# Kernel optimization log

Hardware: AMD Instinct MI355X
Metric: run time of the kernel (lower is better)

## Reference

```python
import jax, jax.numpy as jnp
import numpy as np

B, N, D_MODEL, H = 4, 2048, 1024, 16  # batch, seq, model dim, heads


def setup_inputs() -> dict:
    key = jax.random.key(0)
    k1, k2, k3 = jax.random.split(key, 3)
    x = jax.random.normal(k1, (B, N, D_MODEL), dtype=jnp.float32)
    # nn.Linear weights: [out_features, in_features]; scaled for stability
    Wqkv = jax.random.normal(k2, (3 * D_MODEL, D_MODEL), dtype=jnp.float32) * 0.02
    bqkv = jnp.zeros((3 * D_MODEL,), dtype=jnp.float32)
    Wo = jax.random.normal(k3, (D_MODEL, D_MODEL), dtype=jnp.float32) * 0.02
    bo = jnp.zeros((D_MODEL,), dtype=jnp.float32)
    return {"x": x, "Wqkv": Wqkv, "bqkv": bqkv, "Wo": Wo, "bo": bo}


def reference(x, Wqkv, bqkv, Wo, bo):
    b, n, _ = x.shape
    qkv = x @ Wqkv.T + bqkv                      # [b, n, 3*d_model]
    # rearrange 'b n (h d) -> b h n d' with h heads, then chunk into q,k,v
    qkv = qkv.reshape(b, n, H, -1).transpose(0, 2, 1, 3)  # [b, h, n, 3*dh]
    q, k, v = jnp.split(qkv, 3, axis=-1)          # each [b, h, n, dh]
    scale = k.shape[-1] ** 0.5
    scores = jnp.einsum('bhqd,bhkd->bhqk', q, k) / scale
    attn = jax.nn.softmax(scores, axis=-1)
    out = jnp.einsum('bhqk,bhkd->bhqd', attn, v)  # [b, h, n, dh]
    out = out.transpose(0, 2, 1, 3).reshape(b, n, -1)  # 'b h n d -> b n (h d)'
    return out @ Wo.T + bo
```

## Files before the change

kernel.cpp:

```cpp
#include <hip/hip_runtime.h>
#include <hip/hip_bf16.h>

using bf16 = __hip_bfloat16;
typedef __attribute__((ext_vector_type(8))) __bf16 bf16x8;
typedef __attribute__((ext_vector_type(4))) float f32x4;
typedef __attribute__((ext_vector_type(16))) float f32x16;
typedef __attribute__((ext_vector_type(4))) unsigned u32x4;

#define MFMA16(a, b, c) __builtin_amdgcn_mfma_f32_16x16x32_bf16((a), (b), (c), 0, 0, 0)
#define MFMA32(a, b, c) __builtin_amdgcn_mfma_f32_32x32x16_bf16((a), (b), (c), 0, 0, 0)

#define WAITV4 asm volatile("s_waitcnt vmcnt(4)" ::: "memory")
#define WAITV2 asm volatile("s_waitcnt vmcnt(2)" ::: "memory")
#define WAITV0 asm volatile("s_waitcnt vmcnt(0)" ::: "memory")
#define WAITL0 asm volatile("s_waitcnt lgkmcnt(0)" ::: "memory")
#define BAR    __builtin_amdgcn_s_barrier()
#define SCHED0 __builtin_amdgcn_sched_barrier(0)

static __device__ __forceinline__ void gload_lds16(const bf16* g, bf16* l) {
    __builtin_amdgcn_global_load_lds(
        (__attribute__((address_space(1))) void*)(bf16*)(g),
        (__attribute__((address_space(3))) void*)(l), 16, 0, 0);
}

static __device__ __forceinline__ unsigned cvtpk(float lo, float hi) {
    unsigned r;
    asm("v_cvt_pk_bf16_f32 %0, %1, %2" : "=v"(r) : "v"(lo), "v"(hi));
    return r;
}

__global__ void cvt_all(const float* __restrict__ x, const float* __restrict__ wq,
                        const float* __restrict__ wo,
                        bf16* __restrict__ xb, bf16* __restrict__ wqb, bf16* __restrict__ wob) {
    int b = blockIdx.x;
    const float* src;
    bf16* dst;
    long i;
    if (b < 8192)       { src = x;  dst = xb;  i = (long)b * 256 + threadIdx.x; }
    else if (b < 11264) { src = wq; dst = wqb; i = (long)(b - 8192) * 256 + threadIdx.x; }
    else                { src = wo; dst = wob; i = (long)(b - 11264) * 256 + threadIdx.x; }
    float4 v = ((const float4*)src)[i];
    bf16 t[4];
    t[0] = __float2bfloat16(v.x);
    t[1] = __float2bfloat16(v.y);
    t[2] = __float2bfloat16(v.z);
    t[3] = __float2bfloat16(v.w);
    *(uint2*)(dst + 4l * i) = *(uint2*)t;
}


#define GEMM_STAGE(AB, BB, K0)                                             \
    do {                                                                   \
        gload_lds16(Ab + (long)srow * K + (K0) + scol, (AB) + t * 8);      \
        gload_lds16(Ab + (long)(srow + 64) * K + (K0) + scol, (AB) + 2048 + t * 8); \
        gload_lds16(Bb + (long)srow * K + (K0) + scol, (BB) + t * 8);      \
        gload_lds16(Bb + (long)(srow + 64) * K + (K0) + scol, (BB) + 2048 + t * 8); \
    } while (0)

#define GEMM_COMPUTE(AB, BB)                                               \
    do {                                                                   \
        bf16x8 af[4], bfv[4];                                              \
        _Pragma("unroll") for (int mi4 = 0; mi4 < 4; mi4++)                \
            af[mi4] = *(const bf16x8*)((AB) + (wm * 64 + mi4 * 16 + r) * 32 + q * 8); \
        _Pragma("unroll") for (int ni4 = 0; ni4 < 4; ni4++)                \
            bfv[ni4] = *(const bf16x8*)((BB) + (wn * 64 + ni4 * 16 + r) * 32 + q * 8); \
        __builtin_amdgcn_s_setprio(1);                                     \
        _Pragma("unroll") for (int mi4 = 0; mi4 < 4; mi4++)                \
            _Pragma("unroll") for (int ni4 = 0; ni4 < 4; ni4++)            \
                acc[mi4][ni4] = MFMA16(af[mi4], bfv[ni4], acc[mi4][ni4]);  \
        __builtin_amdgcn_s_setprio(0);                                     \
    } while (0)

#define GEMM_MAIN_LOOP                                                     \
    GEMM_STAGE(A0, B0, 0);                                                 \
    GEMM_STAGE(A1, B1, 32);                                                \
    for (int k0 = 0; k0 < K - 64; k0 += 64) {                              \
        WAITV4; BAR; SCHED0;                                               \
        GEMM_COMPUTE(A0, B0);                                              \
        WAITL0; BAR; SCHED0;                                               \
        GEMM_STAGE(A0, B0, k0 + 64);                                       \
        WAITV4; BAR; SCHED0;                                               \
        GEMM_COMPUTE(A1, B1);                                              \
        WAITL0; BAR; SCHED0;                                               \
        if (k0 + 96 < K) GEMM_STAGE(A1, B1, k0 + 96);                      \
    }                                                                      \
    WAITV4; BAR; SCHED0;                                                   \
    GEMM_COMPUTE(A0, B0);                                                  \
    WAITV0; BAR; SCHED0;                                                   \
    GEMM_COMPUTE(A1, B1);

__global__ void gemm_qkv(const bf16* __restrict__ A, const bf16* __restrict__ B,
                         const float* __restrict__ bias,
                         bf16* __restrict__ Qo, bf16* __restrict__ Ko, bf16* __restrict__ Vt) {
    const int K = 1024;
    __shared__ bf16 smem[16384];
    bf16* A0 = smem;
    bf16* B0 = smem + 4096;
    bf16* A1 = smem + 8192;
    bf16* B1 = smem + 12288;
    int t = threadIdx.x;
    int lane = t & 63;
    int wave = t >> 6;
    int wm = wave >> 1, wn = wave & 1;
    int r = lane & 15, q = lane >> 4;
    int lin = blockIdx.x;
    int xcd = lin & 7, rr_ = lin >> 3;
    int mi = xcd * 8 + rr_ / 24;
    int ni = rr_ % 24;
    long m0 = (long)mi * 128;
    long n0 = (long)ni * 128;
    const bf16* Ab = A + m0 * K;
    const bf16* Bb = B + n0 * K;

    f32x4 acc[4][4] = {};

    int srow = t >> 2;
    int scol = (t & 3) << 3;

    GEMM_MAIN_LOOP

#pragma unroll
    for (int ni4 = 0; ni4 < 4; ni4++) {
        int n = (int)n0 + wn * 64 + ni4 * 16 + r;
        float bn = bias[n];
        int h = n / 192;
        int rem = n % 192;
        int part = rem >> 6;
        int d = rem & 63;
#pragma unroll
        for (int mi4 = 0; mi4 < 4; mi4++) {
#pragma unroll
            for (int rr = 0; rr < 4; rr++) {
                int m = (int)m0 + wm * 64 + mi4 * 16 + q * 4 + rr;
                int b = m >> 11;
                int row = m & 2047;
                long bh = b * 16 + h;
                bf16 bv = __float2bfloat16(acc[mi4][ni4][rr] + bn);
                if (part == 0)      Qo[(bh * 2048 + row) * 64 + d] = bv;
                else if (part == 1) Ko[(bh * 2048 + row) * 64 + d] = bv;
                else                Vt[(bh * 64 + d) * 2048 + row] = bv;
            }
        }
    }
}


#define PACK8(S, OFF, OUTV) { \
    unsigned A0_ = cvtpk(S[OFF+0], S[OFF+1]); \
    unsigned B0_ = cvtpk(S[OFF+4], S[OFF+5]); \
    unsigned A1_ = cvtpk(S[OFF+2], S[OFF+3]); \
    unsigned B1_ = cvtpk(S[OFF+6], S[OFF+7]); \
    asm("v_permlane32_swap_b32 %0, %1" : "+v"(A0_), "+v"(B0_)); \
    asm("v_permlane32_swap_b32 %0, %1" : "+v"(A1_), "+v"(B1_)); \
    u32x4 W; W.x = A0_; W.y = A1_; W.z = B0_; W.w = B1_; \
    OUTV = __builtin_bit_cast(bf16x8, W); }

#define COMPUTE(KB, VB) do { \
    f32x16 sA = {}, sB = {}; \
    __builtin_amdgcn_s_setprio(1); \
    { \
        bf16x8 kA, kB; \
        kA = *(const bf16x8*)(KB + (0 * 64 + lane) * 8); \
        kB = *(const bf16x8*)(KB + (256 + 0 * 64 + lane) * 8); \
        sA = MFMA32(kA, qf0, sA);  sB = MFMA32(kB, qf0, sB); \
        kA = *(const bf16x8*)(KB + (1 * 64 + lane) * 8); \
        kB = *(const bf16x8*)(KB + (256 + 1 * 64 + lane) * 8); \
        sA = MFMA32(kA, qf1, sA);  sB = MFMA32(kB, qf1, sB); \
        kA = *(const bf16x8*)(KB + (2 * 64 + lane) * 8); \
        kB = *(const bf16x8*)(KB + (256 + 2 * 64 + lane) * 8); \
        sA = MFMA32(kA, qf2, sA);  sB = MFMA32(kB, qf2, sB); \
        kA = *(const bf16x8*)(KB + (3 * 64 + lane) * 8); \
        kB = *(const bf16x8*)(KB + (256 + 3 * 64 + lane) * 8); \
        sA = MFMA32(kA, qf3, sA);  sB = MFMA32(kB, qf3, sB); \
    } \
    __builtin_amdgcn_s_setprio(0); \
    float x0 = fmaxf(fmaxf(sA[0], sA[1]), fmaxf(sA[2], sA[3])); \
    float x1 = fmaxf(fmaxf(sA[4], sA[5]), fmaxf(sA[6], sA[7])); \
    float x2 = fmaxf(fmaxf(sA[8], sA[9]), fmaxf(sA[10], sA[11])); \
    float x3 = fmaxf(fmaxf(sA[12], sA[13]), fmaxf(sA[14], sA[15])); \
    float y0 = fmaxf(fmaxf(sB[0], sB[1]), fmaxf(sB[2], sB[3])); \
    float y1 = fmaxf(fmaxf(sB[4], sB[5]), fmaxf(sB[6], sB[7])); \
    float y2 = fmaxf(fmaxf(sB[8], sB[9]), fmaxf(sB[10], sB[11])); \
    float y3 = fmaxf(fmaxf(sB[12], sB[13]), fmaxf(sB[14], sB[15])); \
    float pm = fmaxf(fmaxf(fmaxf(x0, x1), fmaxf(x2, x3)), \
                     fmaxf(fmaxf(y0, y1), fmaxf(y2, y3))); \
    pm = fmaxf(pm, __shfl_xor(pm, 32)); \
    bool resc = !__all(pm <= mv + 8.0f); \
    if (resc) { \
        float mn = fmaxf(mv, pm); \
        float al = __builtin_amdgcn_exp2f((mv - mn) * C1); \
        mv = mn; \
        lv *= al; \
        _Pragma("unroll") for (int e = 0; e < 16; ++e) { o0[e] *= al; o1[e] *= al; } \
    } \
    float mc = mv * C1; \
    _Pragma("unroll") for (int e = 0; e < 16; ++e) sA[e] = __builtin_amdgcn_exp2f(sA[e] * C1 - mc); \
    _Pragma("unroll") for (int e = 0; e < 16; ++e) sB[e] = __builtin_amdgcn_exp2f(sB[e] * C1 - mc); \
    { \
        f32x16 scv = sA + sB; \
        float u0 = (scv[0] + scv[1]) + (scv[2] + scv[3]); \
        float u1 = (scv[4] + scv[5]) + (scv[6] + scv[7]); \
        float u2 = (scv[8] + scv[9]) + (scv[10] + scv[11]); \
        float u3 = (scv[12] + scv[13]) + (scv[14] + scv[15]); \
        float ts = (u0 + u1) + (u2 + u3); \
        ts += __shfl_xor(ts, 32); \
        lv += ts; \
    } \
    bf16x8 pf0, pf1, pf2, pf3; \
    PACK8(sA, 0, pf0); PACK8(sA, 8, pf1); PACK8(sB, 0, pf2); PACK8(sB, 8, pf3); \
    __builtin_amdgcn_s_setprio(1); \
    { \
        bf16x8 vA, vB; \
        vA = *(const bf16x8*)(VB + (0 * 64 + lane) * 8); \
        vB = *(const bf16x8*)(VB + (256 + 0 * 64 + lane) * 8); \
        o0 = MFMA32(vA, pf0, o0);  o1 = MFMA32(vB, pf0, o1); \
        vA = *(const bf16x8*)(VB + (1 * 64 + lane) * 8); \
        vB = *(const bf16x8*)(VB + (256 + 1 * 64 + lane) * 8); \
        o0 = MFMA32(vA, pf1, o0);  o1 = MFMA32(vB, pf1, o1); \
        vA = *(const bf16x8*)(VB + (2 * 64 + lane) * 8); \
        vB = *(const bf16x8*)(VB + (256 + 2 * 64 + lane) * 8); \
        o0 = MFMA32(vA, pf2, o0);  o1 = MFMA32(vB, pf2, o1); \
        vA = *(const bf16x8*)(VB + (3 * 64 + lane) * 8); \
        vB = *(const bf16x8*)(VB + (256 + 3 * 64 + lane) * 8); \
        o0 = MFMA32(vA, pf3, o0);  o1 = MFMA32(vB, pf3, o1); \
    } \
    __builtin_amdgcn_s_setprio(0); \
} while (0)

__global__ __launch_bounds__(512, 4) void attn_fwd(const bf16* __restrict__ Q,
                                                   const bf16* __restrict__ Kg,
                                                   const bf16* __restrict__ Vt,
                                                   bf16* __restrict__ AO) {
    __shared__ bf16 smem[16384];
    bf16* K0 = smem;
    bf16* V0 = smem + 4096;
    bf16* K1 = smem + 8192;
    bf16* V1 = smem + 12288;
    const int t = threadIdx.x;
    const int lane = t & 63, wave = t >> 6;
    const int l31 = lane & 31, hi = lane >> 5;
    const int bid = blockIdx.x;
    const int xcd = bid & 7, idx = bid >> 3;
    const int bh = xcd * 8 + (idx >> 3);
    const int qt = idx & 7;
    const float C1 = 0.18033688011112042f;

    bf16x8 qf0, qf1, qf2, qf3;
    {
        const bf16* Qb = Q + ((long)bh * 2048 + qt * 256 + wave * 32 + l31) * 64 + hi * 8;
        qf0 = *(const bf16x8*)(Qb + 0);
        qf1 = *(const bf16x8*)(Qb + 16);
        qf2 = *(const bf16x8*)(Qb + 32);
        qf3 = *(const bf16x8*)(Qb + 48);
    }

    const bf16* Kh = Kg + (long)bh * 2048 * 64;
    const bf16* Vh = Vt + (long)bh * 64 * 2048;

    const int sr = ((t >> 8) << 5) + (t & 31);
    const int sc = ((t >> 6) & 3) * 16 + ((t >> 5) & 1) * 8;

    f32x16 o0 = {}, o1 = {};
    float mv = -1e30f, lv = 0.f;

    auto issue_stage = [&](bf16* Kb, bf16* Vb, int kv0) {
        gload_lds16(Kh + (long)(kv0 + sr) * 64 + sc, Kb + t * 8);
        gload_lds16(Vh + (long)sr * 2048 + kv0 + sc, Vb + t * 8);
    };

    issue_stage(K0, V0, 0);
    issue_stage(K1, V1, 64);

    for (int kv0 = 0; kv0 < 2048 - 128; kv0 += 128) {
        WAITV2; BAR; SCHED0;
        COMPUTE(K0, V0);
        WAITL0; BAR; SCHED0;
        issue_stage(K0, V0, kv0 + 128);
        WAITV2; BAR; SCHED0;
        COMPUTE(K1, V1);
        WAITL0; BAR; SCHED0;
        if (kv0 + 192 < 2048) issue_stage(K1, V1, kv0 + 192);
    }
    WAITV2; BAR; SCHED0;
    COMPUTE(K0, V0);
    WAITV0; BAR; SCHED0;
    COMPUTE(K1, V1);

    long bb = bh >> 4, hh = bh & 15;
    __syncthreads();
    float il = 1.f / lv;
    char* wbase = (char*)smem + wave * 4096 + l31 * 128;
#pragma unroll
    for (int j = 0; j < 4; ++j) {
        unsigned wlo = cvtpk(o0[4 * j] * il, o0[4 * j + 1] * il);
        unsigned whi = cvtpk(o0[4 * j + 2] * il, o0[4 * j + 3] * il);
        int b8 = 2 * j + hi;
        int b8s = b8 ^ ((l31 & 7) << 1);
        uint2 val; val.x = wlo; val.y = whi;
        *(uint2*)(wbase + b8s * 8) = val;
    }
#pragma unroll
    for (int j = 0; j < 4; ++j) {
        unsigned wlo = cvtpk(o1[4 * j] * il, o1[4 * j + 1] * il);
        unsigned whi = cvtpk(o1[4 * j + 2] * il, o1[4 * j + 3] * il);
        int b8 = 8 + 2 * j + hi;
        int b8s = b8 ^ ((l31 & 7) << 1);
        uint2 val; val.x = wlo; val.y = whi;
        *(uint2*)(wbase + b8s * 8) = val;
    }
    __syncthreads();
    {
        int rid = t >> 1, hf = t & 1;
        int wv = rid >> 5, qq = rid & 31;
        long orow = (long)qt * 256 + wv * 32 + qq;
        const char* rbase = (const char*)smem + wv * 4096 + qq * 128;
        bf16* dst = AO + (bb * 2048 + orow) * 1024 + hh * 64 + hf * 32;
#pragma unroll
        for (int k = 0; k < 4; ++k) {
            int b8 = hf * 8 + 2 * k;
            int b8s = b8 ^ ((qq & 7) << 1);
            int4 v = *(const int4*)(rbase + b8s * 8);
            *(int4*)(dst + k * 8) = v;
        }
    }
}

__global__ void gemm_out(const bf16* __restrict__ A, const bf16* __restrict__ B,
                         const float* __restrict__ bias, float* __restrict__ C) {
    const int K = 1024, N = 1024;
    __shared__ bf16 smem[16384];
    bf16* A0 = smem;
    bf16* B0 = smem + 4096;
    bf16* A1 = smem + 8192;
    bf16* B1 = smem + 12288;
    int t = threadIdx.x;
    int lane = t & 63;
    int wave = t >> 6;
    int wm = wave >> 1, wn = wave & 1;
    int r = lane & 15, q = lane >> 4;
    int lin = blockIdx.x;
    int xcd = lin & 7, rr_ = lin >> 3;
    int mi = xcd * 8 + (rr_ >> 3);
    int ni = rr_ & 7;
    long m0 = (long)mi * 128;
    long n0 = (long)ni * 128;
    const bf16* Ab = A + m0 * K;
    const bf16* Bb = B + n0 * K;

    f32x4 acc[4][4] = {};

    int srow = t >> 2;
    int scol = (t & 3) << 3;

    GEMM_MAIN_LOOP

#pragma unroll
    for (int ni4 = 0; ni4 < 4; ni4++) {
        int n = (int)n0 + wn * 64 + ni4 * 16 + r;
        float bn = bias[n];
#pragma unroll
        for (int mi4 = 0; mi4 < 4; mi4++) {
#pragma unroll
            for (int rr = 0; rr < 4; rr++) {
                long m = m0 + wm * 64 + mi4 * 16 + q * 4 + rr;
                C[m * N + n] = acc[mi4][ni4][rr] + bn;
            }
        }
    }
}

extern "C" void kernel_launch(void* const* d_in, const int* in_sizes, int n_in,
                              void* d_out, int out_size, void* d_ws, size_t ws_size,
                              hipStream_t stream) {
    const float* x    = (const float*)d_in[0];
    const float* Wqkv = (const float*)d_in[1];
    const float* bqkv = (const float*)d_in[2];
    const float* Wo   = (const float*)d_in[3];
    const float* bo   = (const float*)d_in[4];
    float* out = (float*)d_out;

    char* ws = (char*)d_ws;
    bf16* Xb  = (bf16*)(ws + 0);
    bf16* Wqb = (bf16*)(ws + 16777216);
    bf16* Wob = (bf16*)(ws + 23068672);
    bf16* Qb  = (bf16*)(ws + 25165824);
    bf16* Kb  = (bf16*)(ws + 41943040);
    bf16* Vtb = (bf16*)(ws + 58720256);
    bf16* AOb = (bf16*)(ws + 75497472);

    cvt_all<<<12288, 256, 0, stream>>>(x, Wqkv, Wo, Xb, Wqb, Wob);

    gemm_qkv<<<1536, 256, 0, stream>>>(Xb, Wqb, bqkv, Qb, Kb, Vtb);
    attn_fwd<<<512, 512, 0, stream>>>(Qb, Kb, Vtb, AOb);
    gemm_out<<<512, 256, 0, stream>>>(AOb, Wob, bo, out);
}
```

Measured before the change: 202.0 us.

## Double-buffer attention K/V in 128-key chunks with fewer barriers

Shared memory for the attention kernel is doubled so that each pipeline buffer holds two 64-key K/V tiles. The next 128-key chunk is prefetched while the current one is computed, which cuts the number of barrier and wait points per iteration. The explicit partial vmcnt waits are replaced by plain __syncthreads, which waits for all outstanding loads. Launch bounds drop from 4 to 2 blocks per CU, giving the compiler more registers but lowering occupancy because of the larger LDS footprint.

Measured after the change: 215.3 us. 1.07x slower.

```diff
diff --git a/kernel.cpp b/kernel.cpp
--- a/kernel.cpp
+++ b/kernel.cpp
@@ -11,7 +11,6 @@
 #define MFMA32(a, b, c) __builtin_amdgcn_mfma_f32_32x32x16_bf16((a), (b), (c), 0, 0, 0)
 
 #define WAITV4 asm volatile("s_waitcnt vmcnt(4)" ::: "memory")
-#define WAITV2 asm volatile("s_waitcnt vmcnt(2)" ::: "memory")
 #define WAITV0 asm volatile("s_waitcnt vmcnt(0)" ::: "memory")
 #define WAITL0 asm volatile("s_waitcnt lgkmcnt(0)" ::: "memory")
 #define BAR    __builtin_amdgcn_s_barrier()
@@ -47,7 +46,6 @@
     t[3] = __float2bfloat16(v.w);
     *(uint2*)(dst + 4l * i) = *(uint2*)t;
 }
-
 
 #define GEMM_STAGE(AB, BB, K0)                                             \
     do {                                                                   \
@@ -227,15 +225,19 @@
     __builtin_amdgcn_s_setprio(0); \
 } while (0)
 
-__global__ __launch_bounds__(512, 4) void attn_fwd(const bf16* __restrict__ Q,
+__global__ __launch_bounds__(512, 2) void attn_fwd(const bf16* __restrict__ Q,
                                                    const bf16* __restrict__ Kg,
                                                    const bf16* __restrict__ Vt,
                                                    bf16* __restrict__ AO) {
-    __shared__ bf16 smem[16384];
-    bf16* K0 = smem;
-    bf16* V0 = smem + 4096;
-    bf16* K1 = smem + 8192;
-    bf16* V1 = smem + 12288;
+    __shared__ bf16 smem[32768];
+    bf16* K0a = smem;
+    bf16* V0a = smem + 4096;
+    bf16* K0b = smem + 8192;
+    bf16* V0b = smem + 12288;
+    bf16* K1a = smem + 16384;
+    bf16* V1a = smem + 20480;
+    bf16* K1b = smem + 24576;
+    bf16* V1b = smem + 28672;
     const int t = threadIdx.x;
     const int lane = t & 63, wave = t >> 6;
     const int l31 = lane & 31, hi = lane >> 5;
@@ -268,23 +270,25 @@
         gload_lds16(Vh + (long)sr * 2048 + kv0 + sc, Vb + t * 8);
     };
 
-    issue_stage(K0, V0, 0);
-    issue_stage(K1, V1, 64);
-
-    for (int kv0 = 0; kv0 < 2048 - 128; kv0 += 128) {
-        WAITV2; BAR; SCHED0;
-        COMPUTE(K0, V0);
-        WAITL0; BAR; SCHED0;
-        issue_stage(K0, V0, kv0 + 128);
-        WAITV2; BAR; SCHED0;
-        COMPUTE(K1, V1);
-        WAITL0; BAR; SCHED0;
-        if (kv0 + 192 < 2048) issue_stage(K1, V1, kv0 + 192);
-    }
-    WAITV2; BAR; SCHED0;
-    COMPUTE(K0, V0);
-    WAITV0; BAR; SCHED0;
-    COMPUTE(K1, V1);
+    issue_stage(K0a, V0a, 0);
+    issue_stage(K0b, V0b, 64);
+    __syncthreads();
+
+    for (int kv0 = 0;; kv0 += 256) {
+        issue_stage(K1a, V1a, kv0 + 128);
+        issue_stage(K1b, V1b, kv0 + 192);
+        COMPUTE(K0a, V0a);
+        COMPUTE(K0b, V0b);
+        __syncthreads();
+        if (kv0 + 256 < 2048) {
+            issue_stage(K0a, V0a, kv0 + 256);
+            issue_stage(K0b, V0b, kv0 + 320);
+        }
+        COMPUTE(K1a, V1a);
+        COMPUTE(K1b, V1b);
+        if (kv0 + 256 >= 2048) break;
+        __syncthreads();
+    }
 
     long bb = bh >> 4, hh = bh & 15;
     __syncthreads();
```

## Halve attention block size to 128 query rows and simplify double-buffer sync

Applied to the files above, without the earlier changes.

The attention kernel now launches 1024 blocks of 256 threads, each covering 128 query rows instead of 256, so there are more, smaller blocks to spread across CUs. Each thread now issues two async K/V LDS loads per stage. The hand-tuned vmcnt waits and raw barriers are replaced by a simpler prefetch-next-then-compute loop synchronised with __syncthreads. The trade-off is more global/L2 traffic for K/V, since each tile is reused by fewer query rows, and coarser full waits at each barrier.

Result: slower. 206.2 us (+2.1%).

```diff
diff --git a/kernel.cpp b/kernel.cpp
--- a/kernel.cpp
+++ b/kernel.cpp
@@ -11,7 +11,6 @@
 #define MFMA32(a, b, c) __builtin_amdgcn_mfma_f32_32x32x16_bf16((a), (b), (c), 0, 0, 0)
 
 #define WAITV4 asm volatile("s_waitcnt vmcnt(4)" ::: "memory")
-#define WAITV2 asm volatile("s_waitcnt vmcnt(2)" ::: "memory")
 #define WAITV0 asm volatile("s_waitcnt vmcnt(0)" ::: "memory")
 #define WAITL0 asm volatile("s_waitcnt lgkmcnt(0)" ::: "memory")
 #define BAR    __builtin_amdgcn_s_barrier()
@@ -47,7 +46,6 @@
     t[3] = __float2bfloat16(v.w);
     *(uint2*)(dst + 4l * i) = *(uint2*)t;
 }
-
 
 #define GEMM_STAGE(AB, BB, K0)                                             \
     do {                                                                   \
@@ -227,7 +225,7 @@
     __builtin_amdgcn_s_setprio(0); \
 } while (0)
 
-__global__ __launch_bounds__(512, 4) void attn_fwd(const bf16* __restrict__ Q,
+__global__ __launch_bounds__(256, 4) void attn_fwd(const bf16* __restrict__ Q,
                                                    const bf16* __restrict__ Kg,
                                                    const bf16* __restrict__ Vt,
                                                    bf16* __restrict__ AO) {
@@ -241,13 +239,13 @@
     const int l31 = lane & 31, hi = lane >> 5;
     const int bid = blockIdx.x;
     const int xcd = bid & 7, idx = bid >> 3;
-    const int bh = xcd * 8 + (idx >> 3);
-    const int qt = idx & 7;
+    const int bh = xcd * 8 + (idx >> 4);
+    const int qt = idx & 15;
     const float C1 = 0.18033688011112042f;
 
     bf16x8 qf0, qf1, qf2, qf3;
     {
-        const bf16* Qb = Q + ((long)bh * 2048 + qt * 256 + wave * 32 + l31) * 64 + hi * 8;
+        const bf16* Qb = Q + ((long)bh * 2048 + qt * 128 + wave * 32 + l31) * 64 + hi * 8;
         qf0 = *(const bf16x8*)(Qb + 0);
         qf1 = *(const bf16x8*)(Qb + 16);
         qf2 = *(const bf16x8*)(Qb + 32);
@@ -257,34 +255,32 @@
     const bf16* Kh = Kg + (long)bh * 2048 * 64;
     const bf16* Vh = Vt + (long)bh * 64 * 2048;
 
-    const int sr = ((t >> 8) << 5) + (t & 31);
-    const int sc = ((t >> 6) & 3) * 16 + ((t >> 5) & 1) * 8;
-
     f32x16 o0 = {}, o1 = {};
     float mv = -1e30f, lv = 0.f;
 
     auto issue_stage = [&](bf16* Kb, bf16* Vb, int kv0) {
-        gload_lds16(Kh + (long)(kv0 + sr) * 64 + sc, Kb + t * 8);
-        gload_lds16(Vh + (long)sr * 2048 + kv0 + sc, Vb + t * 8);
+#pragma unroll
+        for (int c = 0; c < 2; ++c) {
+            int s = c * 256 + t;
+            int sr = ((s >> 8) << 5) + (s & 31);
+            int sc = ((s >> 6) & 3) * 16 + ((s >> 5) & 1) * 8;
+            gload_lds16(Kh + (long)(kv0 + sr) * 64 + sc, Kb + s * 8);
+            gload_lds16(Vh + (long)sr * 2048 + kv0 + sc, Vb + s * 8);
+        }
     };
 
     issue_stage(K0, V0, 0);
-    issue_stage(K1, V1, 64);
-
-    for (int kv0 = 0; kv0 < 2048 - 128; kv0 += 128) {
-        WAITV2; BAR; SCHED0;
+    __syncthreads();
+
+    for (int kv0 = 0;; kv0 += 128) {
+        issue_stage(K1, V1, kv0 + 64);
         COMPUTE(K0, V0);
-        WAITL0; BAR; SCHED0;
-        issue_stage(K0, V0, kv0 + 128);
-        WAITV2; BAR; SCHED0;
+        __syncthreads();
+        if (kv0 + 128 < 2048) issue_stage(K0, V0, kv0 + 128);
         COMPUTE(K1, V1);
-        WAITL0; BAR; SCHED0;
-        if (kv0 + 192 < 2048) issue_stage(K1, V1, kv0 + 192);
-    }
-    WAITV2; BAR; SCHED0;
-    COMPUTE(K0, V0);
-    WAITV0; BAR; SCHED0;
-    COMPUTE(K1, V1);
+        if (kv0 + 128 >= 2048) break;
+        __syncthreads();
+    }
 
     long bb = bh >> 4, hh = bh & 15;
     __syncthreads();
@@ -312,7 +308,7 @@
     {
         int rid = t >> 1, hf = t & 1;
         int wv = rid >> 5, qq = rid & 31;
-        long orow = (long)qt * 256 + wv * 32 + qq;
+        long orow = (long)qt * 128 + wv * 32 + qq;
         const char* rbase = (const char*)smem + wv * 4096 + qq * 128;
         bf16* dst = AO + (bb * 2048 + orow) * 1024 + hh * 64 + hf * 32;
 #pragma unroll
@@ -391,6 +387,6 @@
     cvt_all<<<12288, 256, 0, stream>>>(x, Wqkv, Wo, Xb, Wqb, Wob);
 
     gemm_qkv<<<1536, 256, 0, stream>>>(Xb, Wqb, bqkv, Qb, Kb, Vtb);
-    attn_fwd<<<512, 512, 0, stream>>>(Qb, Kb, Vtb, AOb);
+    attn_fwd<<<1024, 256, 0, stream>>>(Qb, Kb, Vtb, AOb);
     gemm_out<<<512, 256, 0, stream>>>(AOb, Wob, bo, out);
 }
```

## Restructure attention KV pipeline, fuse softmax row-sum, and reorder GEMM tile mapping

Applied to the files above, without the earlier changes.

The attention KV loop drops the explicit vmcnt waits and raw barriers in favour of __syncthreads. Each iteration now issues the next stage's loads just before computing the current stage. The softmax exp and row-sum are merged into one loop, which replaces the separate tree reduction with a serial accumulation. Both GEMMs switch tile mapping so consecutive blocks within an XCD vary the M tile first, which changes L2 reuse of A versus B. The simpler synchronisation may force full vmcnt(0) waits at each barrier, and the serial sum lengthens the dependency chain.

After: 193.1 us. -4.4%, faster.

```diff
diff --git a/kernel.cpp b/kernel.cpp
--- a/kernel.cpp
+++ b/kernel.cpp
@@ -11,7 +11,6 @@
 #define MFMA32(a, b, c) __builtin_amdgcn_mfma_f32_32x32x16_bf16((a), (b), (c), 0, 0, 0)
 
 #define WAITV4 asm volatile("s_waitcnt vmcnt(4)" ::: "memory")
-#define WAITV2 asm volatile("s_waitcnt vmcnt(2)" ::: "memory")
 #define WAITV0 asm volatile("s_waitcnt vmcnt(0)" ::: "memory")
 #define WAITL0 asm volatile("s_waitcnt lgkmcnt(0)" ::: "memory")
 #define BAR    __builtin_amdgcn_s_barrier()
@@ -48,7 +47,6 @@
     *(uint2*)(dst + 4l * i) = *(uint2*)t;
 }
 
-
 #define GEMM_STAGE(AB, BB, K0)                                             \
     do {                                                                   \
         gload_lds16(Ab + (long)srow * K + (K0) + scol, (AB) + t * 8);      \
@@ -105,8 +103,8 @@
     int r = lane & 15, q = lane >> 4;
     int lin = blockIdx.x;
     int xcd = lin & 7, rr_ = lin >> 3;
-    int mi = xcd * 8 + rr_ / 24;
-    int ni = rr_ % 24;
+    int mi = xcd * 8 + (rr_ & 7);
+    int ni = rr_ >> 3;
     long m0 = (long)mi * 128;
     long n0 = (long)ni * 128;
     const bf16* Ab = A + m0 * K;
@@ -194,18 +192,11 @@
         _Pragma("unroll") for (int e = 0; e < 16; ++e) { o0[e] *= al; o1[e] *= al; } \
     } \
     float mc = mv * C1; \
-    _Pragma("unroll") for (int e = 0; e < 16; ++e) sA[e] = __builtin_amdgcn_exp2f(sA[e] * C1 - mc); \
-    _Pragma("unroll") for (int e = 0; e < 16; ++e) sB[e] = __builtin_amdgcn_exp2f(sB[e] * C1 - mc); \
-    { \
-        f32x16 scv = sA + sB; \
-        float u0 = (scv[0] + scv[1]) + (scv[2] + scv[3]); \
-        float u1 = (scv[4] + scv[5]) + (scv[6] + scv[7]); \
-        float u2 = (scv[8] + scv[9]) + (scv[10] + scv[11]); \
-        float u3 = (scv[12] + scv[13]) + (scv[14] + scv[15]); \
-        float ts = (u0 + u1) + (u2 + u3); \
-        ts += __shfl_xor(ts, 32); \
-        lv += ts; \
-    } \
+    float ts = 0.f; \
+    _Pragma("unroll") for (int e = 0; e < 16; ++e) { float p = __builtin_amdgcn_exp2f(sA[e] * C1 - mc); sA[e] = p; ts += p; } \
+    _Pragma("unroll") for (int e = 0; e < 16; ++e) { float p = __builtin_amdgcn_exp2f(sB[e] * C1 - mc); sB[e] = p; ts += p; } \
+    ts += __shfl_xor(ts, 32); \
+    lv += ts; \
     bf16x8 pf0, pf1, pf2, pf3; \
     PACK8(sA, 0, pf0); PACK8(sA, 8, pf1); PACK8(sB, 0, pf2); PACK8(sB, 8, pf3); \
     __builtin_amdgcn_s_setprio(1); \
@@ -269,22 +260,17 @@
     };
 
     issue_stage(K0, V0, 0);
-    issue_stage(K1, V1, 64);
-
-    for (int kv0 = 0; kv0 < 2048 - 128; kv0 += 128) {
-        WAITV2; BAR; SCHED0;
+    __syncthreads();
+
+    for (int kv0 = 0;; kv0 += 128) {
+        issue_stage(K1, V1, kv0 + 64);
         COMPUTE(K0, V0);
-        WAITL0; BAR; SCHED0;
-        issue_stage(K0, V0, kv0 + 128);
-        WAITV2; BAR; SCHED0;
+        __syncthreads();
+        if (kv0 + 128 < 2048) issue_stage(K0, V0, kv0 + 128);
         COMPUTE(K1, V1);
-        WAITL0; BAR; SCHED0;
-        if (kv0 + 192 < 2048) issue_stage(K1, V1, kv0 + 192);
-    }
-    WAITV2; BAR; SCHED0;
-    COMPUTE(K0, V0);
-    WAITV0; BAR; SCHED0;
-    COMPUTE(K1, V1);
+        if (kv0 + 128 >= 2048) break;
+        __syncthreads();
+    }
 
     long bb = bh >> 4, hh = bh & 15;
     __syncthreads();
@@ -340,8 +326,8 @@
     int r = lane & 15, q = lane >> 4;
     int lin = blockIdx.x;
     int xcd = lin & 7, rr_ = lin >> 3;
-    int mi = xcd * 8 + (rr_ >> 3);
-    int ni = rr_ & 7;
+    int mi = xcd * 8 + (rr_ & 7);
+    int ni = rr_ >> 3;
     long m0 = (long)mi * 128;
     long n0 = (long)ni * 128;
     const bf16* Ab = A + m0 * K;
```
